# Kernel optimization log

Measured on AMD Instinct MI355X. Metric: run time of the kernel, lower is better.

Reference implementation:

```python
import jax, jax.numpy as jnp
import numpy as np

N_GRAPHS = 64   # number of graphs in the batch
H = 128         # hidden dim
L = 3           # num_conv_layers
OUT = 64        # out_feature


def setup_inputs() -> dict:
    key = jax.random.key(0)
    ks = jax.random.split(key, 12)
    N, E, R, C = 10000, 160000, 2, 2
    s = 1.0 / np.sqrt(H)
    inp = {
        'x': jax.random.normal(ks[0], (N, H), jnp.float32),
        'edge_attr': jax.random.normal(ks[1], (E, H), jnp.float32),
        'node_mask': jax.random.uniform(ks[2], (R, C, N, 1), jnp.float32),
        'bond_W': jax.random.normal(ks[3], (L, H, H), jnp.float32) * s,
        'bond_b': jnp.zeros((L, H), jnp.float32),
        'eps': jnp.zeros((L,), jnp.float32),
        'conv_W1': jax.random.normal(ks[4], (L, H, H), jnp.float32) * s,
        'conv_b1': jnp.zeros((L, H), jnp.float32),
        'conv_W2': jax.random.normal(ks[5], (L, H, H), jnp.float32) * s,
        'conv_b2': jnp.zeros((L, H), jnp.float32),
        'mlp_W1': jax.random.normal(ks[6], (H, H), jnp.float32) * s,
        'mlp_b1': jnp.zeros((H,), jnp.float32),
        'mlp_W2': jax.random.normal(ks[7], (H, OUT), jnp.float32) * s,
        'mlp_b2': jnp.zeros((OUT,), jnp.float32),
        'edge_index': jax.random.randint(ks[8], (2, E), 0, N),
        'batch': jnp.sort(jax.random.randint(ks[9], (N,), 0, N_GRAPHS)),
    }
    return inp


def reference(x, edge_attr, node_mask, bond_W, bond_b, eps,
              conv_W1, conv_b1, conv_W2, conv_b2,
              mlp_W1, mlp_b1, mlp_W2, mlp_b2,
              edge_index, batch):
    gelu = lambda v: jax.nn.gelu(v, approximate=False)  # torch exact gelu
    R, C, N, _ = node_mask.shape
    src, dst = edge_index[0], edge_index[1]
    # edge_mask[r,c,e] = node_mask[r,c,src[e]] * node_mask[r,c,dst[e]]
    edge_mask = node_mask[:, :, src, :] * node_mask[:, :, dst, :]  # [R,C,E,1]
    # replica-offset graph ids: [R*C*N]
    batch_full = jnp.tile(batch, R * C) + jnp.repeat(jnp.arange(R * C), N) * N_GRAPHS
    # x repeated over (R, C): [R,C,N,H]
    h = jnp.broadcast_to(x[None, None], (R, C, N, x.shape[-1]))
    for i in range(L):
        emb = edge_attr @ bond_W[i] + bond_b[i]                    # [E,H]
        msg = gelu(h[:, :, src, :] + emb[None, None]) * edge_mask  # [R,C,E,H]
        agg = jnp.zeros_like(h).at[:, :, dst, :].add(msg)          # scatter_sum
        out = (1.0 + eps[i]) * h + agg
        out = gelu(out @ conv_W1[i] + conv_b1[i]) @ conv_W2[i] + conv_b2[i]
        h = gelu(out)  # norm=Identity, dropout=0
    hf = h.reshape(-1, h.shape[-1])                               # [R*C*N,H]
    y = gelu(hf @ mlp_W1 + mlp_b1) @ mlp_W2 + mlp_b2              # [R*C*N,OUT]
    fm = node_mask.reshape(-1, 1)
    D = R * N_GRAPHS * C
    num = jax.ops.segment_sum(y * fm, batch_full, num_segments=D)
    den = jax.ops.segment_sum(fm, batch_full, num_segments=D)
    return num / jnp.maximum(den, 1e-12)
```

## Files before the change

### kernel.cpp

```cpp
#include <hip/hip_runtime.h>

constexpr int H    = 128;
constexpr int NN   = 10000;
constexpr int EE   = 160000;
constexpr int RCN  = 4;
constexpr int NG   = 64;
constexpr int OUTF = 64;
constexpr int DSEG = 256;

using short8 = __attribute__((ext_vector_type(8))) short;
using f32x4  = __attribute__((ext_vector_type(4))) float;

__device__ __forceinline__ float gelu_f(float x){
  float z  = x*0.70710678118654752440f;
  float az = fabsf(z);
  float t  = __builtin_amdgcn_rcpf(fmaf(az, 0.3275911f, 1.0f));
  float e  = __expf(-z*z);
  float poly = fmaf(fmaf(fmaf(fmaf(1.061405429f, t, -1.453152027f),
                              t, 1.421413741f),
                         t, -0.284496736f),
                    t, 0.254829592f) * t;
  float er = fmaf(-poly, e, 1.0f);
  er = copysignf(er, z);
  return 0.5f*x*(1.0f + er);
}

__device__ __forceinline__ void split2(float x, unsigned short& h, unsigned short& m){
  unsigned int u = __float_as_uint(x);
  unsigned int rh = u + 0x7FFF + ((u>>16)&1);
  h = (unsigned short)(rh>>16);
  float fh = __uint_as_float((unsigned int)h << 16);
  float r1 = x - fh;
  unsigned int u1 = __float_as_uint(r1);
  unsigned int rm = u1 + 0x7FFF + ((u1>>16)&1);
  m = (unsigned short)(rm>>16);
}

__device__ __forceinline__ unsigned short bf16rne(float x){
  unsigned int u = __float_as_uint(x);
  return (unsigned short)((u + 0x7FFF + ((u>>16)&1))>>16);
}
__device__ __forceinline__ float bf2f(unsigned short v){
  return __uint_as_float((unsigned int)v << 16);
}

__global__ void k_hist(const int* __restrict__ dst, int* __restrict__ cnt){
  int e = blockIdx.x*256 + threadIdx.x;
  if(e < EE) atomicAdd(&cnt[dst[e]], 1);
}

__global__ __launch_bounds__(1024) void k_scan(const int* __restrict__ cnt,
                                               int* __restrict__ rs, int* __restrict__ cur){
  __shared__ int part[1024];
  int t = threadIdx.x;
  const int CH = 10;
  int base = t*CH;
  int s = 0;
  #pragma unroll
  for(int j=0;j<CH;j++){ int i = base+j; if(i<NN) s += cnt[i]; }
  part[t] = s;
  __syncthreads();
  for(int off=1; off<1024; off<<=1){
    int v = (t>=off) ? part[t-off] : 0;
    __syncthreads();
    part[t] += v;
    __syncthreads();
  }
  int run = (t==0) ? 0 : part[t-1];
  #pragma unroll
  for(int j=0;j<CH;j++){
    int i = base+j;
    if(i<NN){ rs[i] = run; cur[i] = run; run += cnt[i]; }
  }
  if(t == 1023) rs[NN] = part[1023];
}

__global__ void k_fill(const int* __restrict__ dst,
                       int* __restrict__ cur, int* __restrict__ eid){
  int e = blockIdx.x*256 + threadIdx.x;
  if(e >= EE) return;
  int p = atomicAdd(&cur[dst[e]], 1);
  eid[p] = e;
}

__global__ __launch_bounds__(256) void k_sortcsr(const int* __restrict__ rs, int* __restrict__ eid,
                          const int* __restrict__ src, int* __restrict__ esrc){
  int wid  = (blockIdx.x*256 + threadIdx.x) >> 6;
  int lane = threadIdx.x & 63;
  if(wid >= NN) return;
  int jb = rs[wid], je = rs[wid+1];
  int deg = je - jb;
  if(deg <= 0) return;
  if(deg == 1){
    if(lane == 0) esrc[jb] = src[eid[jb]];
    return;
  }
  if(deg <= 64){
    int v = (lane < deg) ? eid[jb + lane] : 0x7FFFFFFF;
    #pragma unroll
    for(int k=2; k<=64; k<<=1){
      #pragma unroll
      for(int j=k>>1; j>0; j>>=1){
        int o = __shfl_xor(v, j, 64);
        bool desc  = (lane & k) != 0;
        bool lower = (lane & j) == 0;
        v = ((lower != desc) ? min(v,o) : max(v,o));
      }
    }
    if(lane < deg){
      eid[jb+lane]  = v;
      esrc[jb+lane] = src[v];
    }
  } else if(lane == 0){
    for(int j=jb+1; j<je; j++){
      int v = eid[j];
      int k = j-1;
      while(k >= jb && eid[k] > v){ eid[k+1] = eid[k]; k--; }
      eid[k+1] = v;
    }
    for(int j=jb; j<je; j++) esrc[j] = src[eid[j]];
  }
}

__global__ void k_gbounds(const int* __restrict__ batch, int* __restrict__ gs){
  int g = threadIdx.x;
  if(g > NG) return;
  if(g == NG){ gs[NG] = NN; return; }
  int lo = 0, hi = NN;
  while(lo < hi){
    int mid = (lo+hi)>>1;
    if(batch[mid] < g) lo = mid+1; else hi = mid;
  }
  gs[g] = lo;
}

__global__ void k_emaskp(const int* __restrict__ src, const int* __restrict__ dst,
                         const int* __restrict__ eid, const float* __restrict__ nm,
                         float4* __restrict__ em4p){
  int j = blockIdx.x*256 + threadIdx.x;
  if(j >= EE) return;
  int e = eid[j];
  int s = src[e], d = dst[e];
  float4 m;
  m.x = nm[0*NN+s]*nm[0*NN+d];
  m.y = nm[1*NN+s]*nm[1*NN+d];
  m.z = nm[2*NN+s]*nm[2*NN+d];
  m.w = nm[3*NN+s]*nm[3*NN+d];
  em4p[j] = m;
}

__global__ void k_splitW(const float* __restrict__ W, unsigned short* __restrict__ oh,
                         unsigned short* __restrict__ om, int nmat, int N){
  int tid = blockIdx.x*256 + threadIdx.x;
  int total = nmat*128*N;
  if(tid >= total) return;
  int mat = tid / (128*N);
  int rem = tid - mat*(128*N);
  int k = rem / N;
  int n = rem - k*N;
  int NF = N >> 4;
  int ks = k >> 5, kk = k & 31;
  int nf = n >> 4;
  int lane = (n & 15) + 16*((kk & 15) >> 2);
  int e = 4*(kk >> 4) + (kk & 3);
  size_t idx = (size_t)mat*128*N + ((size_t)(ks*NF + nf)*64 + lane)*8 + e;
  unsigned short hh, mm;
  split2(W[tid], hh, mm);
  oh[idx] = hh; om[idx] = mm;
}

__global__ void k_splitA(const float* __restrict__ A, const int* __restrict__ eid,
                         unsigned short* __restrict__ oh){
  int tid = blockIdx.x*256 + threadIdx.x;
  if(tid >= EE*32) return;
  int j = tid >> 5, kq = tid & 31;
  int k = kq*4;
  int rsrc = eid[j];
  float4 v = *(const float4*)&A[(size_t)rsrc*H + k];
  ushort4 hh;
  hh.x = bf16rne(v.x); hh.y = bf16rne(v.y);
  hh.z = bf16rne(v.z); hh.w = bf16rne(v.w);
  *(ushort4*)&oh[(size_t)j*H + k] = hh;
}

template<int NFO, bool A2, bool GELU, int OMODE>
__global__ __launch_bounds__(256) void k_sgemm(
    const unsigned short* __restrict__ Ah, const unsigned short* __restrict__ Am,
    const unsigned short* __restrict__ Wh, const unsigned short* __restrict__ Wm,
    const float* __restrict__ bias, float* __restrict__ Cf,
    unsigned short* __restrict__ Oh, unsigned short* __restrict__ Om, int nrows){
  int t = threadIdx.x;
  int w = t >> 6, lane = t & 63;
  int m15 = lane & 15, kg = lane >> 4;
  int rowbase = blockIdx.x*128;

  const int SMAX = 4*NFO - 1;
  auto ldW = [&](int s, short8* d){
    size_t widx = ((size_t)s*64 + lane)*8;
    d[0] = *(const short8*)&Wh[widx];
    d[1] = *(const short8*)&Wm[widx];
  };

  int arow[2];
  #pragma unroll
  for(int mf=0;mf<2;mf++){
    int r = rowbase + w*32 + mf*16 + m15;
    arow[mf] = (r < nrows) ? r : (nrows-1);
  }

  f32x4 acc[2][NFO];
  #pragma unroll
  for(int mf=0;mf<2;mf++)
    #pragma unroll
    for(int nf=0;nf<NFO;nf++) acc[mf][nf] = (f32x4){0.f,0.f,0.f,0.f};

  short8 cw[2], nw[2];
  ldW(0, cw);
  ldW(1 <= SMAX ? 1 : SMAX, nw);

  for(int ks=0;ks<4;ks++){
    short8 ah[2], am[2];
    #pragma unroll
    for(int mf=0;mf<2;mf++){
      size_t base = (size_t)arow[mf]*H + ks*32 + kg*4;
      ushort4 hlo = *(const ushort4*)&Ah[base];
      ushort4 hhi = *(const ushort4*)&Ah[base + 16];
      ah[mf] = (short8){(short)hlo.x,(short)hlo.y,(short)hlo.z,(short)hlo.w,
                        (short)hhi.x,(short)hhi.y,(short)hhi.z,(short)hhi.w};
      if(A2){
        ushort4 mlo = *(const ushort4*)&Am[base];
        ushort4 mhi = *(const ushort4*)&Am[base + 16];
        am[mf] = (short8){(short)mlo.x,(short)mlo.y,(short)mlo.z,(short)mlo.w,
                          (short)mhi.x,(short)mhi.y,(short)mhi.z,(short)mhi.w};
      }
    }
    #pragma unroll
    for(int nf=0;nf<NFO;nf++){
      int s = ks*NFO + nf;
      short8 pw[2];
      ldW(s+2 <= SMAX ? s+2 : SMAX, pw);
      #pragma unroll
      for(int mf=0;mf<2;mf++){
        acc[mf][nf] = __builtin_amdgcn_mfma_f32_16x16x32_bf16(ah[mf], cw[0], acc[mf][nf], 0,0,0);
        acc[mf][nf] = __builtin_amdgcn_mfma_f32_16x16x32_bf16(ah[mf], cw[1], acc[mf][nf], 0,0,0);
        if(A2)
          acc[mf][nf] = __builtin_amdgcn_mfma_f32_16x16x32_bf16(am[mf], cw[0], acc[mf][nf], 0,0,0);
      }
      cw[0]=nw[0]; cw[1]=nw[1];
      nw[0]=pw[0]; nw[1]=pw[1];
    }
  }
  #pragma unroll
  for(int mf=0;mf<2;mf++){
    #pragma unroll
    for(int nf=0;nf<NFO;nf++){
      int gcol = nf*16 + m15;
      float bv = bias[gcol];
      #pragma unroll
      for(int r=0;r<4;r++){
        int grow = rowbase + w*32 + mf*16 + kg*4 + r;
        if(grow >= nrows) continue;
        float v = acc[mf][nf][r] + bv;
        if(GELU) v = gelu_f(v);
        size_t idx = (size_t)grow*(NFO*16) + gcol;
        if(OMODE == 0) Cf[idx] = v;
        if(OMODE == 1){
          unsigned short hh, mm2;
          split2(v, hh, mm2);
          Oh[idx] = hh; Om[idx] = mm2;
        }
        if(OMODE == 2) Oh[idx] = bf16rne(v);
      }
    }
  }
}

template<int NFO2, bool G2, int OMODE>
__global__ __launch_bounds__(256) void k_fuse2(
    const unsigned short* __restrict__ Ah, const unsigned short* __restrict__ Am,
    const unsigned short* __restrict__ W1h, const unsigned short* __restrict__ W1m,
    const float* __restrict__ b1,
    const unsigned short* __restrict__ W2h, const unsigned short* __restrict__ W2m,
    const float* __restrict__ b2,
    float* __restrict__ Cf,
    unsigned short* __restrict__ Oh, unsigned short* __restrict__ Om, int nrows){
  __shared__ unsigned int Ul[4*32*132];
  int t = threadIdx.x;
  int w = t >> 6, lane = t & 63;
  int m15 = lane & 15, kg = lane >> 4;
  int rowbase = blockIdx.x*128;
  unsigned int* Uw = &Ul[w*32*132];

  int arow[2];
  #pragma unroll
  for(int mf=0;mf<2;mf++){
    int r = rowbase + w*32 + mf*16 + m15;
    arow[mf] = (r < nrows) ? r : (nrows-1);
  }

  {
    const int SMAX = 31;
    auto ldW = [&](int s, short8* d){
      size_t widx = ((size_t)s*64 + lane)*8;
      d[0] = *(const short8*)&W1h[widx];
      d[1] = *(const short8*)&W1m[widx];
    };
    f32x4 acc[2][8];
    #pragma unroll
    for(int mf=0;mf<2;mf++)
      #pragma unroll
      for(int nf=0;nf<8;nf++) acc[mf][nf] = (f32x4){0.f,0.f,0.f,0.f};
    short8 cw[2], nw[2];
    ldW(0, cw); ldW(1, nw);
    for(int ks=0;ks<4;ks++){
      short8 ah[2], am[2];
      #pragma unroll
      for(int mf=0;mf<2;mf++){
        size_t base = (size_t)arow[mf]*H + ks*32 + kg*4;
        ushort4 hlo = *(const ushort4*)&Ah[base];
        ushort4 hhi = *(const ushort4*)&Ah[base + 16];
        ushort4 mlo = *(const ushort4*)&Am[base];
        ushort4 mhi = *(const ushort4*)&Am[base + 16];
        ah[mf] = (short8){(short)hlo.x,(short)hlo.y,(short)hlo.z,(short)hlo.w,
                          (short)hhi.x,(short)hhi.y,(short)hhi.z,(short)hhi.w};
        am[mf] = (short8){(short)mlo.x,(short)mlo.y,(short)mlo.z,(short)mlo.w,
                          (short)mhi.x,(short)mhi.y,(short)mhi.z,(short)mhi.w};
      }
      #pragma unroll
      for(int nf=0;nf<8;nf++){
        int s = ks*8 + nf;
        short8 pw[2];
        ldW(s+2 <= SMAX ? s+2 : SMAX, pw);
        #pragma unroll
        for(int mf=0;mf<2;mf++){
          acc[mf][nf] = __builtin_amdgcn_mfma_f32_16x16x32_bf16(ah[mf], cw[0], acc[mf][nf], 0,0,0);
          acc[mf][nf] = __builtin_amdgcn_mfma_f32_16x16x32_bf16(ah[mf], cw[1], acc[mf][nf], 0,0,0);
          acc[mf][nf] = __builtin_amdgcn_mfma_f32_16x16x32_bf16(am[mf], cw[0], acc[mf][nf], 0,0,0);
        }
        cw[0]=nw[0]; cw[1]=nw[1];
        nw[0]=pw[0]; nw[1]=pw[1];
      }
    }
    #pragma unroll
    for(int mf=0;mf<2;mf++){
      #pragma unroll
      for(int nf=0;nf<8;nf++){
        float bv = b1[nf*16 + m15];
        #pragma unroll
        for(int r=0;r<4;r++){
          float v = gelu_f(acc[mf][nf][r] + bv);
          unsigned short hh, mm2;
          split2(v, hh, mm2);
          int wrow = mf*16 + kg*4 + r;
          Uw[wrow*132 + nf*16 + m15] = (unsigned)hh | ((unsigned)mm2 << 16);
        }
      }
    }
  }
  __syncthreads();

  {
    const int SMAX = 4*NFO2 - 1;
    auto ldW = [&](int s, short8* d){
      size_t widx = ((size_t)s*64 + lane)*8;
      d[0] = *(const short8*)&W2h[widx];
      d[1] = *(const short8*)&W2m[widx];
    };
    f32x4 acc[2][NFO2];
    #pragma unroll
    for(int mf=0;mf<2;mf++)
      #pragma unroll
      for(int nf=0;nf<NFO2;nf++) acc[mf][nf] = (f32x4){0.f,0.f,0.f,0.f};
    short8 cw[2], nw[2];
    ldW(0, cw); ldW(1 <= SMAX ? 1 : SMAX, nw);
    for(int ks=0;ks<4;ks++){
      short8 ah[2], am[2];
      #pragma unroll
      for(int mf=0;mf<2;mf++){
        const unsigned int* base = &Uw[(mf*16 + m15)*132 + ks*32 + kg*4];
        uint4 q0 = *(const uint4*)base;
        uint4 q1 = *(const uint4*)(base + 16);
        unsigned h0 = (q0.x & 0xFFFFu) | (q0.y << 16);
        unsigned h1 = (q0.z & 0xFFFFu) | (q0.w << 16);
        unsigned h2 = (q1.x & 0xFFFFu) | (q1.y << 16);
        unsigned h3 = (q1.z & 0xFFFFu) | (q1.w << 16);
        unsigned M0 = (q0.x >> 16) | (q0.y & 0xFFFF0000u);
        unsigned M1 = (q0.z >> 16) | (q0.w & 0xFFFF0000u);
        unsigned M2 = (q1.x >> 16) | (q1.y & 0xFFFF0000u);
        unsigned M3 = (q1.z >> 16) | (q1.w & 0xFFFF0000u);
        union { uint4 u; short8 s; } cvh, cvm;
        cvh.u = (uint4){h0,h1,h2,h3};
        cvm.u = (uint4){M0,M1,M2,M3};
        ah[mf] = cvh.s; am[mf] = cvm.s;
      }
      #pragma unroll
      for(int nf=0;nf<NFO2;nf++){
        int s = ks*NFO2 + nf;
        short8 pw[2];
        ldW(s+2 <= SMAX ? s+2 : SMAX, pw);
        #pragma unroll
        for(int mf=0;mf<2;mf++){
          acc[mf][nf] = __builtin_amdgcn_mfma_f32_16x16x32_bf16(ah[mf], cw[0], acc[mf][nf], 0,0,0);
          acc[mf][nf] = __builtin_amdgcn_mfma_f32_16x16x32_bf16(ah[mf], cw[1], acc[mf][nf], 0,0,0);
          acc[mf][nf] = __builtin_amdgcn_mfma_f32_16x16x32_bf16(am[mf], cw[0], acc[mf][nf], 0,0,0);
        }
        cw[0]=nw[0]; cw[1]=nw[1];
        nw[0]=pw[0]; nw[1]=pw[1];
      }
    }
    #pragma unroll
    for(int mf=0;mf<2;mf++){
      #pragma unroll
      for(int nf=0;nf<NFO2;nf++){
        int gcol = nf*16 + m15;
        float bv = b2[gcol];
        #pragma unroll
        for(int r=0;r<4;r++){
          int grow = rowbase + w*32 + mf*16 + kg*4 + r;
          if(grow >= nrows) continue;
          float v = acc[mf][nf][r] + bv;
          if(G2) v = gelu_f(v);
          size_t idx = (size_t)grow*(NFO2*16) + gcol;
          if(OMODE == 0) Cf[idx] = v;
          if(OMODE == 1){
            unsigned short hh, mm2;
            split2(v, hh, mm2);
            Oh[idx] = hh; Om[idx] = mm2;
          }
        }
      }
    }
  }
}

#define AGG_LD(J, EV, H0, H1, M0, M1) do{                                   \
    int s_ = esrc[(J)];                                                     \
    ushort4 e4_ = *(const ushort4*)&embB[(size_t)(J)*H + d0];               \
    EV.x = bf2f(e4_.x); EV.y = bf2f(e4_.y);                                 \
    EV.z = bf2f(e4_.z); EV.w = bf2f(e4_.w);                                 \
    float4 m_ = em4p[(J)];                                                  \
    M0 = half ? m_.z : m_.x;                                                \
    M1 = half ? m_.w : m_.y;                                                \
    if(FIRST){                                                              \
      H0 = *(const float4*)&hin[(size_t)s_*H + d0];                         \
      H1 = H0;                                                              \
    } else {                                                                \
      H0 = *(const float4*)&hin[((size_t)s_*RCN + rc0)*H + d0];             \
      H1 = *(const float4*)&hin[((size_t)s_*RCN + rc1)*H + d0];             \
    }                                                                       \
  }while(0)

#define AGG_STEP(EV, H0, H1, M0, M1) do{                                    \
    if(FIRST){                                                              \
      float gx = gelu_f(H0.x+EV.x);                                         \
      float gy = gelu_f(H0.y+EV.y);                                         \
      float gz = gelu_f(H0.z+EV.z);                                         \
      float gw = gelu_f(H0.w+EV.w);                                         \
      acc0.x += gx*M0; acc0.y += gy*M0; acc0.z += gz*M0; acc0.w += gw*M0;   \
      acc1.x += gx*M1; acc1.y += gy*M1; acc1.z += gz*M1; acc1.w += gw*M1;   \
    } else {                                                                \
      acc0.x += gelu_f(H0.x+EV.x)*M0;                                       \
      acc0.y += gelu_f(H0.y+EV.y)*M0;                                       \
      acc0.z += gelu_f(H0.z+EV.z)*M0;                                       \
      acc0.w += gelu_f(H0.w+EV.w)*M0;                                       \
      acc1.x += gelu_f(H1.x+EV.x)*M1;                                       \
      acc1.y += gelu_f(H1.y+EV.y)*M1;                                       \
      acc1.z += gelu_f(H1.z+EV.z)*M1;                                       \
      acc1.w += gelu_f(H1.w+EV.w)*M1;                                       \
    }                                                                       \
  }while(0)

template<bool FIRST>
__global__ __launch_bounds__(256) void k_agg(const float* __restrict__ hin,
                       const unsigned short* __restrict__ embB, const float4* __restrict__ em4p,
                       const int* __restrict__ rs, const int* __restrict__ esrc,
                       const float* __restrict__ epsp,
                       unsigned short* __restrict__ Th, unsigned short* __restrict__ Tm){
  int t = threadIdx.x;
  int w = t >> 6;
  int lane = t & 63;
  int half = lane >> 5;
  int l32 = lane & 31;
  int n = blockIdx.x*4 + w;
  int d0 = l32*4;
  int rc0 = half*2, rc1 = rc0+1;
  float4 acc0 = {0.f,0.f,0.f,0.f}, acc1 = {0.f,0.f,0.f,0.f};
  int jb = rs[n], je = rs[n+1];

  float4 ev0, h00, h10, ev1, h01, h11, ev2, h02, h12;
  float  m00, m10, m01, m11, m02, m12;

  if(jb < je){
    AGG_LD(jb, ev0, h00, h10, m00, m10);
    if(jb+1 < je) AGG_LD(jb+1, ev1, h01, h11, m01, m11);
    if(jb+2 < je) AGG_LD(jb+2, ev2, h02, h12, m02, m12);
    int j = jb;
    for(;;){
      AGG_STEP(ev0, h00, h10, m00, m10);
      if(j+3 < je) AGG_LD(j+3, ev0, h00, h10, m00, m10);
      if(++j >= je) break;
      AGG_STEP(ev1, h01, h11, m01, m11);
      if(j+3 < je) AGG_LD(j+3, ev1, h01, h11, m01, m11);
      if(++j >= je) break;
      AGG_STEP(ev2, h02, h12, m02, m12);
      if(j+3 < je) AGG_LD(j+3, ev2, h02, h12, m02, m12);
      if(++j >= je) break;
    }
  }
  float e1 = 1.0f + epsp[0];
  #pragma unroll
  for(int p=0;p<2;p++){
    int rc = p ? rc1 : rc0;
    float4 ac = p ? acc1 : acc0;
    const float* hb = FIRST ? (hin + (size_t)n*H) : (hin + ((size_t)n*RCN + rc)*H);
    float4 hv = *(const float4*)&hb[d0];
    float4 o;
    o.x = e1*hv.x + ac.x; o.y = e1*hv.y + ac.y;
    o.z = e1*hv.z + ac.z; o.w = e1*hv.w + ac.w;
    int row = n*RCN + rc;
    ushort4 hh, mm;
    split2(o.x, hh.x, mm.x);
    split2(o.y, hh.y, mm.y);
    split2(o.z, hh.z, mm.z);
    split2(o.w, hh.w, mm.w);
    size_t idx = (size_t)row*H + d0;
    *(ushort4*)&Th[idx] = hh;
    *(ushort4*)&Tm[idx] = mm;
  }
}

__global__ __launch_bounds__(64) void k_pool(const float* __restrict__ y, const float* __restrict__ nm,
                       const int* __restrict__ gs, float* __restrict__ out){
  int seg = blockIdx.x;
  int rc = seg / NG;
  int g  = seg - rc*NG;
  int c  = threadIdx.x;
  int nb = gs[g], ne = gs[g+1];
  float num = 0.f, den = 0.f;
  for(int n=nb; n<ne; n++){
    float w = nm[rc*NN + n];
    num += y[((size_t)n*RCN + rc)*OUTF + c] * w;
    den += w;
  }
  out[seg*OUTF + c] = num / fmaxf(den, 1e-12f);
}

extern "C" void kernel_launch(void* const* d_in, const int* in_sizes, int n_in,
                              void* d_out, int out_size, void* d_ws, size_t ws_size,
                              hipStream_t stream){
  const float* x         = (const float*)d_in[0];
  const float* edge_attr = (const float*)d_in[1];
  const float* node_mask = (const float*)d_in[2];
  const float* bond_W    = (const float*)d_in[3];
  const float* bond_b    = (const float*)d_in[4];
  const float* epsv      = (const float*)d_in[5];
  const float* conv_W1   = (const float*)d_in[6];
  const float* conv_b1   = (const float*)d_in[7];
  const float* conv_W2   = (const float*)d_in[8];
  const float* conv_b2   = (const float*)d_in[9];
  const float* mlp_W1    = (const float*)d_in[10];
  const float* mlp_b1    = (const float*)d_in[11];
  const float* mlp_W2    = (const float*)d_in[12];
  const float* mlp_b2    = (const float*)d_in[13];
  const int*   eidx      = (const int*)d_in[14];
  const int*   batch     = (const int*)d_in[15];
  const int* srcp = eidx;
  const int* dstp = eidx + EE;

  char* p = (char*)d_ws;
  auto alloc = [&](size_t bytes)->char*{
    char* r = p; p += (bytes + 255) & ~size_t(255); return r;
  };
  float*  h    = (float*) alloc((size_t)RCN*NN*H*4);
  unsigned short* embB = (unsigned short*)alloc((size_t)EE*H*2);
  float4* em4p = (float4*)alloc((size_t)EE*16);
  float*  y    = (float*) alloc((size_t)RCN*NN*OUTF*4);
  int*    cnt  = (int*)   alloc((size_t)NN*4);
  int*    rs   = (int*)   alloc((size_t)(NN+1)*4);
  int*    cur  = (int*)   alloc((size_t)NN*4);
  int*    eid  = (int*)   alloc((size_t)EE*4);
  int*    esrc = (int*)   alloc((size_t)EE*4);
  int*    gs   = (int*)   alloc((size_t)(NG+1)*4);
  unsigned short* WBh  = (unsigned short*)alloc((size_t)3*16384*2);
  unsigned short* WBm  = (unsigned short*)alloc((size_t)3*16384*2);
  unsigned short* WC1h = (unsigned short*)alloc((size_t)3*16384*2);
  unsigned short* WC1m = (unsigned short*)alloc((size_t)3*16384*2);
  unsigned short* WC2h = (unsigned short*)alloc((size_t)3*16384*2);
  unsigned short* WC2m = (unsigned short*)alloc((size_t)3*16384*2);
  unsigned short* WM1h = (unsigned short*)alloc((size_t)16384*2);
  unsigned short* WM1m = (unsigned short*)alloc((size_t)16384*2);
  unsigned short* WM2h = (unsigned short*)alloc((size_t)8192*2);
  unsigned short* WM2m = (unsigned short*)alloc((size_t)8192*2);
  unsigned short* EAh  = (unsigned short*)alloc((size_t)EE*H*2);
  const size_t NPB = (size_t)RCN*NN*H*2;
  unsigned short* TBh = (unsigned short*)alloc(NPB);
  unsigned short* TBm = (unsigned short*)alloc(NPB);
  if((size_t)(p - (char*)d_ws) > ws_size) return;

  hipMemsetAsync(cnt, 0, (size_t)NN*4, stream);

  k_hist    <<<(EE+255)/256, 256, 0, stream>>>(dstp, cnt);
  k_scan    <<<1, 1024, 0, stream>>>(cnt, rs, cur);
  k_fill    <<<(EE+255)/256, 256, 0, stream>>>(dstp, cur, eid);
  k_sortcsr <<<(NN*64+255)/256, 256, 0, stream>>>(rs, eid, srcp, esrc);
  k_emaskp  <<<(EE+255)/256, 256, 0, stream>>>(srcp, dstp, eid, node_mask, em4p);
  k_splitA  <<<EE*32/256, 256, 0, stream>>>(edge_attr, eid, EAh);
  k_gbounds <<<1, 128, 0, stream>>>(batch, gs);
  k_splitW  <<<192, 256, 0, stream>>>(bond_W,  WBh,  WBm,  3, 128);
  k_splitW  <<<192, 256, 0, stream>>>(conv_W1, WC1h, WC1m, 3, 128);
  k_splitW  <<<192, 256, 0, stream>>>(conv_W2, WC2h, WC2m, 3, 128);
  k_splitW  <<<64,  256, 0, stream>>>(mlp_W1,  WM1h, WM1m, 1, 128);
  k_splitW  <<<32,  256, 0, stream>>>(mlp_W2,  WM2h, WM2m, 1, 64);

  const int NROWS = RCN*NN;
  const int GB_E = EE/128;
  const int GB_N = (NROWS+127)/128;
  for(int l=0; l<3; l++){
    size_t wo = (size_t)l*16384;
    k_sgemm<8,false,false,2><<<GB_E, 256, 0, stream>>>(
        EAh, nullptr, WBh+wo, WBm+wo, bond_b + l*H, nullptr, embB, nullptr, EE);
    if(l == 0)
      k_agg<true ><<<NN/4, 256, 0, stream>>>(x, embB, em4p, rs, esrc, epsv + l, TBh, TBm);
    else
      k_agg<false><<<NN/4, 256, 0, stream>>>(h, embB, em4p, rs, esrc, epsv + l, TBh, TBm);
    if(l < 2)
      k_fuse2<8,true,0><<<GB_N, 256, 0, stream>>>(
          TBh, TBm, WC1h+wo, WC1m+wo, conv_b1 + l*H,
          WC2h+wo, WC2m+wo, conv_b2 + l*H, h, nullptr, nullptr, NROWS);
    else
      k_fuse2<8,true,1><<<GB_N, 256, 0, stream>>>(
          TBh, TBm, WC1h+wo, WC1m+wo, conv_b1 + l*H,
          WC2h+wo, WC2m+wo, conv_b2 + l*H, nullptr, TBh, TBm, NROWS);
  }
  k_fuse2<4,false,0><<<GB_N, 256, 0, stream>>>(
      TBh, TBm, WM1h, WM1m, mlp_b1, WM2h, WM2m, mlp_b2,
      y, nullptr, nullptr, NROWS);
  k_pool<<<DSEG, 64, 0, stream>>>(y, node_mask, gs, (float*)d_out);
}
```

Before: 559.0 us.

## Fuse bond-embedding GEMM into aggregation kernel, computing edge embeddings per destination node

Removes the separate edge-embedding GEMM and its bf16 intermediate buffer. Each wave in the aggregation kernel now computes the embedding for its node's incoming edges in groups of 16 with MFMA, stages the results in shared memory, and consumes them in the gather loop. This saves the write and re-read of the E×H embedding each layer. In exchange, MFMA tiles are underused when a node has fewer than 16 edges, weights are reloaded from global per group, and the h-gather prefetch depth drops from three to two.

```diff
diff --git a/kernel.cpp b/kernel.cpp
--- a/kernel.cpp
+++ b/kernel.cpp
@@ -39,9 +39,6 @@
 __device__ __forceinline__ unsigned short bf16rne(float x){
   unsigned int u = __float_as_uint(x);
   return (unsigned short)((u + 0x7FFF + ((u>>16)&1))>>16);
-}
-__device__ __forceinline__ float bf2f(unsigned short v){
-  return __uint_as_float((unsigned int)v << 16);
 }
 
 __global__ void k_hist(const int* __restrict__ dst, int* __restrict__ cnt){
@@ -183,98 +180,6 @@
   *(ushort4*)&oh[(size_t)j*H + k] = hh;
 }
 
-template<int NFO, bool A2, bool GELU, int OMODE>
-__global__ __launch_bounds__(256) void k_sgemm(
-    const unsigned short* __restrict__ Ah, const unsigned short* __restrict__ Am,
-    const unsigned short* __restrict__ Wh, const unsigned short* __restrict__ Wm,
-    const float* __restrict__ bias, float* __restrict__ Cf,
-    unsigned short* __restrict__ Oh, unsigned short* __restrict__ Om, int nrows){
-  int t = threadIdx.x;
-  int w = t >> 6, lane = t & 63;
-  int m15 = lane & 15, kg = lane >> 4;
-  int rowbase = blockIdx.x*128;
-
-  const int SMAX = 4*NFO - 1;
-  auto ldW = [&](int s, short8* d){
-    size_t widx = ((size_t)s*64 + lane)*8;
-    d[0] = *(const short8*)&Wh[widx];
-    d[1] = *(const short8*)&Wm[widx];
-  };
-
-  int arow[2];
-  #pragma unroll
-  for(int mf=0;mf<2;mf++){
-    int r = rowbase + w*32 + mf*16 + m15;
-    arow[mf] = (r < nrows) ? r : (nrows-1);
-  }
-
-  f32x4 acc[2][NFO];
-  #pragma unroll
-  for(int mf=0;mf<2;mf++)
-    #pragma unroll
-    for(int nf=0;nf<NFO;nf++) acc[mf][nf] = (f32x4){0.f,0.f,0.f,0.f};
-
-  short8 cw[2], nw[2];
-  ldW(0, cw);
-  ldW(1 <= SMAX ? 1 : SMAX, nw);
-
-  for(int ks=0;ks<4;ks++){
-    short8 ah[2], am[2];
-    #pragma unroll
-    for(int mf=0;mf<2;mf++){
-      size_t base = (size_t)arow[mf]*H + ks*32 + kg*4;
-      ushort4 hlo = *(const ushort4*)&Ah[base];
-      ushort4 hhi = *(const ushort4*)&Ah[base + 16];
-      ah[mf] = (short8){(short)hlo.x,(short)hlo.y,(short)hlo.z,(short)hlo.w,
-                        (short)hhi.x,(short)hhi.y,(short)hhi.z,(short)hhi.w};
-      if(A2){
-        ushort4 mlo = *(const ushort4*)&Am[base];
-        ushort4 mhi = *(const ushort4*)&Am[base + 16];
-        am[mf] = (short8){(short)mlo.x,(short)mlo.y,(short)mlo.z,(short)mlo.w,
-                          (short)mhi.x,(short)mhi.y,(short)mhi.z,(short)mhi.w};
-      }
-    }
-    #pragma unroll
-    for(int nf=0;nf<NFO;nf++){
-      int s = ks*NFO + nf;
-      short8 pw[2];
-      ldW(s+2 <= SMAX ? s+2 : SMAX, pw);
-      #pragma unroll
-      for(int mf=0;mf<2;mf++){
-        acc[mf][nf] = __builtin_amdgcn_mfma_f32_16x16x32_bf16(ah[mf], cw[0], acc[mf][nf], 0,0,0);
-        acc[mf][nf] = __builtin_amdgcn_mfma_f32_16x16x32_bf16(ah[mf], cw[1], acc[mf][nf], 0,0,0);
-        if(A2)
-          acc[mf][nf] = __builtin_amdgcn_mfma_f32_16x16x32_bf16(am[mf], cw[0], acc[mf][nf], 0,0,0);
-      }
-      cw[0]=nw[0]; cw[1]=nw[1];
-      nw[0]=pw[0]; nw[1]=pw[1];
-    }
-  }
-  #pragma unroll
-  for(int mf=0;mf<2;mf++){
-    #pragma unroll
-    for(int nf=0;nf<NFO;nf++){
-      int gcol = nf*16 + m15;
-      float bv = bias[gcol];
-      #pragma unroll
-      for(int r=0;r<4;r++){
-        int grow = rowbase + w*32 + mf*16 + kg*4 + r;
-        if(grow >= nrows) continue;
-        float v = acc[mf][nf][r] + bv;
-        if(GELU) v = gelu_f(v);
-        size_t idx = (size_t)grow*(NFO*16) + gcol;
-        if(OMODE == 0) Cf[idx] = v;
-        if(OMODE == 1){
-          unsigned short hh, mm2;
-          split2(v, hh, mm2);
-          Oh[idx] = hh; Om[idx] = mm2;
-        }
-        if(OMODE == 2) Oh[idx] = bf16rne(v);
-      }
-    }
-  }
-}
-
 template<int NFO2, bool G2, int OMODE>
 __global__ __launch_bounds__(256) void k_fuse2(
     const unsigned short* __restrict__ Ah, const unsigned short* __restrict__ Am,
@@ -433,11 +338,8 @@
   }
 }
 
-#define AGG_LD(J, EV, H0, H1, M0, M1) do{                                   \
+#define LDH(J, H0, H1, M0, M1) do{                                          \
     int s_ = esrc[(J)];                                                     \
-    ushort4 e4_ = *(const ushort4*)&embB[(size_t)(J)*H + d0];               \
-    EV.x = bf2f(e4_.x); EV.y = bf2f(e4_.y);                                 \
-    EV.z = bf2f(e4_.z); EV.w = bf2f(e4_.w);                                 \
     float4 m_ = em4p[(J)];                                                  \
     M0 = half ? m_.z : m_.x;                                                \
     M1 = half ? m_.w : m_.y;                                                \
@@ -472,41 +374,81 @@
 
 template<bool FIRST>
 __global__ __launch_bounds__(256) void k_agg(const float* __restrict__ hin,
-                       const unsigned short* __restrict__ embB, const float4* __restrict__ em4p,
+                       const unsigned short* __restrict__ EAh,
+                       const unsigned short* __restrict__ Wh, const unsigned short* __restrict__ Wm,
+                       const float* __restrict__ bb,
+                       const float4* __restrict__ em4p,
                        const int* __restrict__ rs, const int* __restrict__ esrc,
                        const float* __restrict__ epsp,
                        unsigned short* __restrict__ Th, unsigned short* __restrict__ Tm){
+  __shared__ float Ebuf[4][16*132];
   int t = threadIdx.x;
   int w = t >> 6;
   int lane = t & 63;
   int half = lane >> 5;
   int l32 = lane & 31;
+  int m15 = lane & 15, kg = lane >> 4;
   int n = blockIdx.x*4 + w;
   int d0 = l32*4;
   int rc0 = half*2, rc1 = rc0+1;
+  float* Ew = Ebuf[w];
   float4 acc0 = {0.f,0.f,0.f,0.f}, acc1 = {0.f,0.f,0.f,0.f};
   int jb = rs[n], je = rs[n+1];
 
-  float4 ev0, h00, h10, ev1, h01, h11, ev2, h02, h12;
-  float  m00, m10, m01, m11, m02, m12;
-
+  float bias_v[8];
+  #pragma unroll
+  for(int nf=0;nf<8;nf++) bias_v[nf] = bb[nf*16 + m15];
+
+  float4 hA0, hA1, hB0, hB1;
+  float  mA0, mA1, mB0, mB1;
   if(jb < je){
-    AGG_LD(jb, ev0, h00, h10, m00, m10);
-    if(jb+1 < je) AGG_LD(jb+1, ev1, h01, h11, m01, m11);
-    if(jb+2 < je) AGG_LD(jb+2, ev2, h02, h12, m02, m12);
-    int j = jb;
-    for(;;){
-      AGG_STEP(ev0, h00, h10, m00, m10);
-      if(j+3 < je) AGG_LD(j+3, ev0, h00, h10, m00, m10);
-      if(++j >= je) break;
-      AGG_STEP(ev1, h01, h11, m01, m11);
-      if(j+3 < je) AGG_LD(j+3, ev1, h01, h11, m01, m11);
-      if(++j >= je) break;
-      AGG_STEP(ev2, h02, h12, m02, m12);
-      if(j+3 < je) AGG_LD(j+3, ev2, h02, h12, m02, m12);
-      if(++j >= je) break;
-    }
-  }
+    LDH(jb, hA0, hA1, mA0, mA1);
+    if(jb+1 < je) LDH(jb+1, hB0, hB1, mB0, mB1);
+  }
+
+  int j = jb;
+  for(int gstart = jb; gstart < je; gstart += 16){
+    int cnt = je - gstart; if(cnt > 16) cnt = 16;
+    {
+      int arow = gstart + m15; if(arow > je-1) arow = je-1;
+      short8 ah[4];
+      #pragma unroll
+      for(int ks=0;ks<4;ks++){
+        size_t base = (size_t)arow*H + ks*32 + kg*4;
+        ushort4 lo = *(const ushort4*)&EAh[base];
+        ushort4 hi = *(const ushort4*)&EAh[base + 16];
+        ah[ks] = (short8){(short)lo.x,(short)lo.y,(short)lo.z,(short)lo.w,
+                          (short)hi.x,(short)hi.y,(short)hi.z,(short)hi.w};
+      }
+      #pragma unroll
+      for(int nf=0;nf<8;nf++){
+        f32x4 acc = (f32x4){0.f,0.f,0.f,0.f};
+        #pragma unroll
+        for(int ks=0;ks<4;ks++){
+          size_t widx = ((size_t)(ks*8 + nf)*64 + lane)*8;
+          short8 wh = *(const short8*)&Wh[widx];
+          short8 wm = *(const short8*)&Wm[widx];
+          acc = __builtin_amdgcn_mfma_f32_16x16x32_bf16(ah[ks], wh, acc, 0,0,0);
+          acc = __builtin_amdgcn_mfma_f32_16x16x32_bf16(ah[ks], wm, acc, 0,0,0);
+        }
+        #pragma unroll
+        for(int r=0;r<4;r++)
+          Ew[(kg*4 + r)*132 + nf*16 + m15] = acc[r] + bias_v[nf];
+      }
+    }
+    for(int jj=0; jj<cnt; jj++){
+      float4 ev = *(const float4*)&Ew[jj*132 + d0];
+      if(((j - jb) & 1) == 0){
+        AGG_STEP(ev, hA0, hA1, mA0, mA1);
+        if(j+2 < je) LDH(j+2, hA0, hA1, mA0, mA1);
+      } else {
+        AGG_STEP(ev, hB0, hB1, mB0, mB1);
+        if(j+2 < je) LDH(j+2, hB0, hB1, mB0, mB1);
+      }
+      j++;
+    }
+  }
+
   float e1 = 1.0f + epsp[0];
   #pragma unroll
   for(int p=0;p<2;p++){
@@ -572,7 +514,6 @@
     char* r = p; p += (bytes + 255) & ~size_t(255); return r;
   };
   float*  h    = (float*) alloc((size_t)RCN*NN*H*4);
-  unsigned short* embB = (unsigned short*)alloc((size_t)EE*H*2);
   float4* em4p = (float4*)alloc((size_t)EE*16);
   float*  y    = (float*) alloc((size_t)RCN*NN*OUTF*4);
   int*    cnt  = (int*)   alloc((size_t)NN*4);
@@ -613,16 +554,15 @@
   k_splitW  <<<32,  256, 0, stream>>>(mlp_W2,  WM2h, WM2m, 1, 64);
 
   const int NROWS = RCN*NN;
-  const int GB_E = EE/128;
   const int GB_N = (NROWS+127)/128;
   for(int l=0; l<3; l++){
     size_t wo = (size_t)l*16384;
-    k_sgemm<8,false,false,2><<<GB_E, 256, 0, stream>>>(
-        EAh, nullptr, WBh+wo, WBm+wo, bond_b + l*H, nullptr, embB, nullptr, EE);
     if(l == 0)
-      k_agg<true ><<<NN/4, 256, 0, stream>>>(x, embB, em4p, rs, esrc, epsv + l, TBh, TBm);
+      k_agg<true ><<<NN/4, 256, 0, stream>>>(x, EAh, WBh+wo, WBm+wo, bond_b + l*H,
+                                             em4p, rs, esrc, epsv + l, TBh, TBm);
     else
-      k_agg<false><<<NN/4, 256, 0, stream>>>(h, embB, em4p, rs, esrc, epsv + l, TBh, TBm);
+      k_agg<false><<<NN/4, 256, 0, stream>>>(h, EAh, WBh+wo, WBm+wo, bond_b + l*H,
+                                             em4p, rs, esrc, epsv + l, TBh, TBm);
     if(l < 2)
       k_fuse2<8,true,0><<<GB_N, 256, 0, stream>>>(
           TBh, TBm, WC1h+wo, WC1m+wo, conv_b1 + l*H,
```

Result: slower. 805.5 us (+44.1%).
